# Kernel optimization log

Hardware: AMD Instinct MI355X
Metric: run time of the kernel (lower is better)

Reference implementation:

```python
import jax, jax.numpy as jnp
import numpy as np

B, N0, C, H, T = 32, 513, 768, 12, 10
Dh = C // H
SCALE = Dh ** -0.5
HID = 4 * C  # mlp hidden


def _ln(x, g, b, eps=1e-5):
    m = jnp.mean(x, axis=-1, keepdims=True)
    v = jnp.mean((x - m) ** 2, axis=-1, keepdims=True)
    return (x - m) * jax.lax.rsqrt(v + eps) * g + b


def setup_inputs() -> dict:
    key = jax.random.key(0)
    ks = jax.random.split(key, 8)
    s = 0.02
    return {
        "x": jax.random.normal(ks[0], (B, N0, C), jnp.float32),
        "global_feature": jax.random.normal(ks[1], (B, 1, C), jnp.float32),
        "token_position": jax.random.normal(ks[2], (T, C), jnp.float32) * s,
        "prompt_emb": jax.random.normal(ks[3], (T, C), jnp.float32) * s,
        "scaler1": jnp.ones((1,), jnp.float32) * 0.3,
        "g1": jnp.ones((C,), jnp.float32),
        "b1": jnp.zeros((C,), jnp.float32),
        "w_qkv": jax.random.normal(ks[4], (3 * C, C), jnp.float32) * s,
        "w_proj": jax.random.normal(ks[5], (C, C), jnp.float32) * s,
        "b_proj": jnp.zeros((C,), jnp.float32),
        "g2": jnp.ones((C,), jnp.float32),
        "b2": jnp.zeros((C,), jnp.float32),
        "w_fc1": jax.random.normal(ks[6], (HID, C), jnp.float32) * s,
        "b_fc1": jnp.zeros((HID,), jnp.float32),
        "w_fc2": jax.random.normal(ks[7], (C, HID), jnp.float32) * s,
        "b_fc2": jnp.zeros((C,), jnp.float32),
    }


def reference(x, global_feature, token_position, prompt_emb, scaler1,
              g1, b1, w_qkv, w_proj, b_proj, g2, b2,
              w_fc1, b_fc1, w_fc2, b_fc2):
    # prompt-token fusion: [1,T,C] + [B,1,C] + [1,T,C] -> [B,T,C]
    token_prompt = prompt_emb[None] + scaler1 * global_feature + token_position[None]
    x = jnp.concatenate([x[:, :1], token_prompt, x[:, 1:]], axis=1)  # [B, N, C]
    Bx, N, _ = x.shape

    # attention branch
    h = _ln(x, g1, b1)
    qkv = h @ w_qkv.T  # [B, N, 3C]
    qkv = qkv.reshape(Bx, N, 3, H, Dh)
    q = qkv[:, :, 0].transpose(0, 2, 1, 3)  # [B, H, N, Dh]
    k = qkv[:, :, 1].transpose(0, 2, 1, 3)
    v = qkv[:, :, 2].transpose(0, 2, 1, 3)
    attn = jax.nn.softmax(jnp.einsum('bhqd,bhkd->bhqk', q, k) * SCALE, axis=-1)
    o = jnp.einsum('bhqk,bhkd->bhqd', attn, v).transpose(0, 2, 1, 3).reshape(Bx, N, C)
    x = x + o @ w_proj.T + b_proj

    # mlp branch (exact GELU as nn.GELU)
    h2 = _ln(x, g2, b2)
    x = x + jax.nn.gelu(h2 @ w_fc1.T + b_fc1, approximate=False) @ w_fc2.T + b_fc2
    return x
```

## Files before the change

kernel.cpp:

```cpp
#include <hip/hip_runtime.h>
#include <math.h>

typedef float  f32x4 __attribute__((ext_vector_type(4)));
typedef short  s16x8 __attribute__((ext_vector_type(8)));
typedef unsigned short u16;

#define DEVI static __device__ __forceinline__

constexpr int B_   = 32, N0_ = 513, C_ = 768, H_ = 12, T_ = 10;
constexpr int NSEQ = 523;
constexpr int M_   = B_ * NSEQ;
constexpr int HID_ = 3072;
constexpr float SCALE_ = 0.125f;
constexpr int NPAD = 576;

constexpr size_t OFF_A  = 25706496;
constexpr size_t OFF_VT = OFF_A + 77119488;
constexpr size_t OFF_O  = OFF_VT + 28311552;
constexpr size_t OFF_W  = OFF_O + 25706496;
constexpr size_t OFF_WQ = OFF_W;
constexpr size_t OFF_WP = OFF_WQ + 3538944;
constexpr size_t OFF_W1 = OFF_WP + 1179648;
constexpr size_t OFF_W2 = OFF_W1 + 4718592;

DEVI u16 f2bf(float f) {
  union { float f; unsigned u; } x; x.f = f;
  unsigned r = x.u + 0x7fffu + ((x.u >> 16) & 1u);
  return (u16)(r >> 16);
}

DEVI void async_ld16(const void* g, void* l) {
  __builtin_amdgcn_global_load_lds(
      (const __attribute__((address_space(1))) unsigned*)g,
      (__attribute__((address_space(3))) unsigned*)l, 16, 0, 0);
}

DEVI f32x4 mfma16(s16x8 a, s16x8 b, f32x4 c) {
  return __builtin_amdgcn_mfma_f32_16x16x32_bf16(a, b, c, 0, 0, 0);
}

__global__ void k_cvt(const float* __restrict__ in, u16* __restrict__ out, int n4) {
  int i = blockIdx.x * 256 + threadIdx.x;
  if (i >= n4) return;
  float4 v = reinterpret_cast<const float4*>(in)[i];
  ushort4 o;
  o.x = f2bf(v.x); o.y = f2bf(v.y); o.z = f2bf(v.z); o.w = f2bf(v.w);
  reinterpret_cast<ushort4*>(out)[i] = o;
}

__global__ void k_build(const float* __restrict__ x, const float* __restrict__ gf,
                        const float* __restrict__ tp, const float* __restrict__ pe,
                        const float* __restrict__ s1, float* __restrict__ xcat) {
  int i = blockIdx.x * 256 + threadIdx.x;
  if (i >= M_ * C_ / 4) return;
  int row = i / (C_ / 4), c4 = i % (C_ / 4);
  int b = row / NSEQ, n = row - b * NSEQ;
  float4 v;
  if (n == 0) {
    v = reinterpret_cast<const float4*>(x + (size_t)b * N0_ * C_)[c4];
  } else if (n <= T_) {
    int t = n - 1;
    float4 a  = reinterpret_cast<const float4*>(pe + (size_t)t * C_)[c4];
    float4 tv = reinterpret_cast<const float4*>(tp + (size_t)t * C_)[c4];
    float4 g  = reinterpret_cast<const float4*>(gf + (size_t)b * C_)[c4];
    float s = s1[0];
    v.x = a.x + s * g.x + tv.x; v.y = a.y + s * g.y + tv.y;
    v.z = a.z + s * g.z + tv.z; v.w = a.w + s * g.w + tv.w;
  } else {
    v = reinterpret_cast<const float4*>(x + ((size_t)b * N0_ + (n - T_)) * C_)[c4];
  }
  reinterpret_cast<float4*>(xcat + (size_t)row * C_)[c4] = v;
}

__global__ void k_ln(const float* __restrict__ xin, const float* __restrict__ g,
                     const float* __restrict__ bb, u16* __restrict__ hout) {
  int lane = threadIdx.x & 63, wid = threadIdx.x >> 6;
  int row = blockIdx.x * 4 + wid;
  const float4* xr = reinterpret_cast<const float4*>(xin + (size_t)row * C_);
  float4 v[3]; float s = 0.f, sq = 0.f;
#pragma unroll
  for (int c = 0; c < 3; ++c) {
    v[c] = xr[c * 64 + lane];
    s  += v[c].x + v[c].y + v[c].z + v[c].w;
    sq += v[c].x * v[c].x + v[c].y * v[c].y + v[c].z * v[c].z + v[c].w * v[c].w;
  }
#pragma unroll
  for (int m = 1; m < 64; m <<= 1) { s += __shfl_xor(s, m, 64); sq += __shfl_xor(sq, m, 64); }
  float mean = s * (1.f / C_);
  float rstd = rsqrtf(sq * (1.f / C_) - mean * mean + 1e-5f);
  ushort4* orow = reinterpret_cast<ushort4*>(hout + (size_t)row * C_);
#pragma unroll
  for (int c = 0; c < 3; ++c) {
    float4 gv = reinterpret_cast<const float4*>(g)[c * 64 + lane];
    float4 bv = reinterpret_cast<const float4*>(bb)[c * 64 + lane];
    ushort4 o;
    o.x = f2bf((v[c].x - mean) * rstd * gv.x + bv.x);
    o.y = f2bf((v[c].y - mean) * rstd * gv.y + bv.y);
    o.z = f2bf((v[c].z - mean) * rstd * gv.z + bv.z);
    o.w = f2bf((v[c].w - mean) * rstd * gv.w + bv.w);
    orow[c * 64 + lane] = o;
  }
}

template<int EPI, int NDIM, int KDIM>
__global__ __launch_bounds__(256) void k_gemm(
    const u16* __restrict__ A, const u16* __restrict__ Bw,
    u16* __restrict__ outb, float* __restrict__ outf,
    const float* __restrict__ bias, const float* __restrict__ resid,
    u16* __restrict__ vT) {
  __shared__ __align__(16) char lds[32768];
  const int m0 = blockIdx.x * 128, n0 = blockIdx.y * 128;
  const int lane = threadIdx.x & 63, wid = threadIdx.x >> 6;
  const int wr = wid >> 1, wc = wid & 1;
  f32x4 acc[4][4] = {};

  for (int k0 = 0; k0 < KDIM; k0 += 64) {
    __syncthreads();
#pragma unroll
    for (int jj = 0; jj < 4; ++jj) {
      int j = wid * 4 + jj;
      int row = j * 8 + (lane >> 3);
      int gm = m0 + row; if (gm > M_ - 1) gm = M_ - 1;
      int cb = ((lane & 7) * 16) ^ ((row & 7) << 4);
      async_ld16((const char*)A + ((size_t)gm * KDIM + k0) * 2 + cb, lds + j * 1024);
    }
#pragma unroll
    for (int jj = 0; jj < 4; ++jj) {
      int j = wid * 4 + jj;
      int row = j * 8 + (lane >> 3);
      int cb = ((lane & 7) * 16) ^ ((row & 7) << 4);
      async_ld16((const char*)Bw + ((size_t)(n0 + row) * KDIM + k0) * 2 + cb,
                 lds + 16384 + j * 1024);
    }
    __syncthreads();
#pragma unroll
    for (int kk = 0; kk < 2; ++kk) {
      s16x8 af[4], bfr[4];
#pragma unroll
      for (int i = 0; i < 4; ++i) {
        int row = wr * 64 + i * 16 + (lane & 15);
        int cb = (kk * 64 + (lane >> 4) * 16) ^ ((row & 7) << 4);
        af[i] = *reinterpret_cast<const s16x8*>(lds + row * 128 + cb);
      }
#pragma unroll
      for (int j = 0; j < 4; ++j) {
        int row = wc * 64 + j * 16 + (lane & 15);
        int cb = (kk * 64 + (lane >> 4) * 16) ^ ((row & 7) << 4);
        bfr[j] = *reinterpret_cast<const s16x8*>(lds + 16384 + row * 128 + cb);
      }
#pragma unroll
      for (int i = 0; i < 4; ++i)
#pragma unroll
        for (int j = 0; j < 4; ++j)
          acc[i][j] = mfma16(af[i], bfr[j], acc[i][j]);
    }
  }

#pragma unroll
  for (int i = 0; i < 4; ++i) {
#pragma unroll
    for (int j = 0; j < 4; ++j) {
#pragma unroll
      for (int r = 0; r < 4; ++r) {
        int gm = m0 + wr * 64 + i * 16 + (lane >> 4) * 4 + r;
        int gn = n0 + wc * 64 + j * 16 + (lane & 15);
        if (gm < M_) {
          float v = acc[i][j][r];
          if constexpr (EPI == 0) {
            u16 bv = f2bf(v);
            outb[(size_t)gm * NDIM + gn] = bv;
            if (gn >= 2 * C_) {
              int hh = (gn - 2 * C_) >> 6;
              int dh = gn & 63;
              int b2 = gm / NSEQ, nn = gm - b2 * NSEQ;
              vT[((size_t)(b2 * H_ + hh) * 64 + dh) * NPAD + nn] = bv;
            }
          } else if constexpr (EPI == 1) {
            size_t idx = (size_t)gm * NDIM + gn;
            outf[idx] = v + bias[gn] + resid[idx];
          } else {
            float t = v + bias[gn];
            outb[(size_t)gm * NDIM + gn] =
                f2bf(0.5f * t * (1.f + erff(t * 0.70710678118654752f)));
          }
        }
      }
    }
  }
}

__global__ __launch_bounds__(256) void k_attn(const u16* __restrict__ qkv,
                                              const u16* __restrict__ vT,
                                              u16* __restrict__ o) {
  __shared__ __align__(16) char lds[24576];
  const int qt = blockIdx.x, bh = blockIdx.y;
  const int b = bh / H_, h = bh - b * H_;
  const int lane = threadIdx.x & 63, wid = threadIdx.x >> 6;

  s16x8 qf[2];
  {
    int n = qt * 64 + wid * 16 + (lane & 15); if (n > NSEQ - 1) n = NSEQ - 1;
    const u16* qrow = qkv + (size_t)(b * NSEQ + n) * (3 * C_) + h * 64 + (lane >> 4) * 8;
    qf[0] = *reinterpret_cast<const s16x8*>(qrow);
    qf[1] = *reinterpret_cast<const s16x8*>(qrow + 32);
  }
  float m_run[4] = {-1e30f, -1e30f, -1e30f, -1e30f};
  float l_run[4] = {0.f, 0.f, 0.f, 0.f};
  f32x4 oacc[4] = {};
  char* pl = lds + 16384 + wid * 2048;

  for (int t = 0; t < 9; ++t) {
    const int kv0 = t * 64;
    __syncthreads();
#pragma unroll
    for (int jj = 0; jj < 2; ++jj) {
      int j = wid * 2 + jj;
      int row = j * 8 + (lane >> 3);
      int n = kv0 + row; if (n > NSEQ - 1) n = NSEQ - 1;
      int cb = ((lane & 7) * 16) ^ ((row & 7) << 4);
      async_ld16((const char*)(qkv + (size_t)(b * NSEQ + n) * (3 * C_) + C_ + h * 64) + cb,
                 lds + j * 1024);
    }
#pragma unroll
    for (int jj = 0; jj < 2; ++jj) {
      int j = wid * 2 + jj;
      int dh = j * 8 + (lane >> 3);
      int cb = ((lane & 7) * 16) ^ ((dh & 7) << 4);
      async_ld16((const char*)(vT + ((size_t)bh * 64 + dh) * NPAD + kv0) + cb,
                 lds + 8192 + j * 1024);
    }
    __syncthreads();

    f32x4 sfr[4] = {};
#pragma unroll
    for (int kk = 0; kk < 2; ++kk) {
#pragma unroll
      for (int fc = 0; fc < 4; ++fc) {
        int row = fc * 16 + (lane & 15);
        int cb = (kk * 64 + (lane >> 4) * 16) ^ ((row & 7) << 4);
        s16x8 kf = *reinterpret_cast<const s16x8*>(lds + row * 128 + cb);
        sfr[fc] = mfma16(qf[kk], kf, sfr[fc]);
      }
    }
#pragma unroll
    for (int fc = 0; fc < 4; ++fc) {
      bool valid = (kv0 + fc * 16 + (lane & 15)) < NSEQ;
#pragma unroll
      for (int r = 0; r < 4; ++r)
        sfr[fc][r] = valid ? sfr[fc][r] * SCALE_ : -1e30f;
    }
#pragma unroll
    for (int r = 0; r < 4; ++r) {
      float mx = fmaxf(fmaxf(sfr[0][r], sfr[1][r]), fmaxf(sfr[2][r], sfr[3][r]));
      mx = fmaxf(mx, __shfl_xor(mx, 1, 64));
      mx = fmaxf(mx, __shfl_xor(mx, 2, 64));
      mx = fmaxf(mx, __shfl_xor(mx, 4, 64));
      mx = fmaxf(mx, __shfl_xor(mx, 8, 64));
      float mnew = fmaxf(m_run[r], mx);
      float sc = __expf(m_run[r] - mnew);
      l_run[r] *= sc;
#pragma unroll
      for (int f2 = 0; f2 < 4; ++f2) oacc[f2][r] *= sc;
      float ps = 0.f;
#pragma unroll
      for (int fc = 0; fc < 4; ++fc) {
        float p = __expf(sfr[fc][r] - mnew);
        sfr[fc][r] = p; ps += p;
      }
      ps += __shfl_xor(ps, 1, 64);
      ps += __shfl_xor(ps, 2, 64);
      ps += __shfl_xor(ps, 4, 64);
      ps += __shfl_xor(ps, 8, 64);
      l_run[r] += ps;
      m_run[r] = mnew;
    }
#pragma unroll
    for (int fc = 0; fc < 4; ++fc)
#pragma unroll
      for (int r = 0; r < 4; ++r) {
        int row = (lane >> 4) * 4 + r;
        int cb = ((fc * 16 + (lane & 15)) * 2) ^ ((row & 7) << 4);
        *reinterpret_cast<u16*>(pl + row * 128 + cb) = f2bf(sfr[fc][r]);
      }
    s16x8 pf[2];
#pragma unroll
    for (int ks = 0; ks < 2; ++ks) {
      int row = lane & 15;
      int cb = (ks * 64 + (lane >> 4) * 16) ^ ((row & 7) << 4);
      pf[ks] = *reinterpret_cast<const s16x8*>(pl + row * 128 + cb);
    }
#pragma unroll
    for (int f2 = 0; f2 < 4; ++f2)
#pragma unroll
      for (int ks = 0; ks < 2; ++ks) {
        int vrow = f2 * 16 + (lane & 15);
        int cb = (ks * 64 + (lane >> 4) * 16) ^ ((vrow & 7) << 4);
        s16x8 vf = *reinterpret_cast<const s16x8*>(lds + 8192 + vrow * 128 + cb);
        oacc[f2] = mfma16(pf[ks], vf, oacc[f2]);
      }
  }
#pragma unroll
  for (int f2 = 0; f2 < 4; ++f2)
#pragma unroll
    for (int r = 0; r < 4; ++r) {
      int n = qt * 64 + wid * 16 + (lane >> 4) * 4 + r;
      if (n < NSEQ) {
        float val = oacc[f2][r] / l_run[r];
        o[(size_t)(b * NSEQ + n) * C_ + h * 64 + f2 * 16 + (lane & 15)] = f2bf(val);
      }
    }
}

extern "C" void kernel_launch(void* const* d_in, const int* in_sizes, int n_in,
                              void* d_out, int out_size, void* d_ws, size_t ws_size,
                              hipStream_t stream) {
  const float* x    = (const float*)d_in[0];
  const float* gf   = (const float*)d_in[1];
  const float* tp   = (const float*)d_in[2];
  const float* pe   = (const float*)d_in[3];
  const float* s1   = (const float*)d_in[4];
  const float* g1   = (const float*)d_in[5];
  const float* b1   = (const float*)d_in[6];
  const float* wqkv = (const float*)d_in[7];
  const float* wproj= (const float*)d_in[8];
  const float* bproj= (const float*)d_in[9];
  const float* g2   = (const float*)d_in[10];
  const float* b2   = (const float*)d_in[11];
  const float* wfc1 = (const float*)d_in[12];
  const float* bfc1 = (const float*)d_in[13];
  const float* wfc2 = (const float*)d_in[14];
  const float* bfc2 = (const float*)d_in[15];

  char* ws = (char*)d_ws;
  u16* h    = (u16*)ws;
  u16* qkvb = (u16*)(ws + OFF_A);
  u16* hmid = qkvb;
  u16* vTb  = (u16*)(ws + OFF_VT);
  u16* ob   = (u16*)(ws + OFF_O);
  u16* wqb  = (u16*)(ws + OFF_WQ);
  u16* wpb  = (u16*)(ws + OFF_WP);
  u16* w1b  = (u16*)(ws + OFF_W1);
  u16* w2b  = (u16*)(ws + OFF_W2);
  float* xcat = (float*)d_out;

  k_cvt<<<(442368 + 255) / 256, 256, 0, stream>>>(wqkv, wqb, 442368);
  k_cvt<<<(147456 + 255) / 256, 256, 0, stream>>>(wproj, wpb, 147456);
  k_cvt<<<(589824 + 255) / 256, 256, 0, stream>>>(wfc1, w1b, 589824);
  k_cvt<<<(589824 + 255) / 256, 256, 0, stream>>>(wfc2, w2b, 589824);

  k_build<<<(M_ * C_ / 4 + 255) / 256, 256, 0, stream>>>(x, gf, tp, pe, s1, xcat);
  k_ln<<<M_ / 4, 256, 0, stream>>>(xcat, g1, b1, h);
  k_gemm<0, 2304, 768><<<dim3(131, 18), 256, 0, stream>>>(h, wqb, qkvb, nullptr, nullptr, nullptr, vTb);
  k_attn<<<dim3(9, B_ * H_), 256, 0, stream>>>(qkvb, vTb, ob);
  k_gemm<1, 768, 768><<<dim3(131, 6), 256, 0, stream>>>(ob, wpb, nullptr, xcat, bproj, xcat, nullptr);
  k_ln<<<M_ / 4, 256, 0, stream>>>(xcat, g2, b2, h);
  k_gemm<2, 3072, 768><<<dim3(131, 24), 256, 0, stream>>>(h, w1b, hmid, nullptr, bfc1, nullptr, nullptr);
  k_gemm<1, 768, 3072><<<dim3(131, 6), 256, 0, stream>>>(hmid, w2b, nullptr, (float*)d_out, bfc2, xcat, nullptr);
}
```

Measured before the change: 882.9 us.

## Enlarge GEMM tiles, double-buffer LDS, and remap workgroups across XCDs

The GEMM kernel now uses templated 256x256 or 256x128 tiles with 512 threads (8 waves), replacing 128x128 tiles with 256 threads. It double-buffers the K-loop in dynamic shared memory so the next tile's global-to-LDS load overlaps the current MFMA work, and it maps workgroup IDs so consecutive tiles land on the same XCD. The goal is more data reuse per loaded tile, hidden memory latency and better L2 locality. The costs are more LDS and registers per block, fewer blocks in flight, and less even wave balance on the tail.

```diff
diff --git a/kernel.cpp b/kernel.cpp
--- a/kernel.cpp
+++ b/kernel.cpp
@@ -102,70 +102,94 @@
   }
 }
 
-template<int EPI, int NDIM, int KDIM>
-__global__ __launch_bounds__(256) void k_gemm(
+template<int EPI, int NDIM, int KDIM, int BM, int BN>
+__global__ __launch_bounds__(512, 2) void k_gemm(
     const u16* __restrict__ A, const u16* __restrict__ Bw,
     u16* __restrict__ outb, float* __restrict__ outf,
     const float* __restrict__ bias, const float* __restrict__ resid,
     u16* __restrict__ vT) {
-  __shared__ __align__(16) char lds[32768];
-  const int m0 = blockIdx.x * 128, n0 = blockIdx.y * 128;
+  extern __shared__ __align__(16) char smem[];
+  constexpr int NMB  = (M_ + BM - 1) / BM;
+  constexpr int MI   = BM / 32;
+  constexpr int NJ   = BN / 64;
+  constexpr int BUFB = (BM + BN) * 128;
+  constexpr int NT   = KDIM / 64;
+
   const int lane = threadIdx.x & 63, wid = threadIdx.x >> 6;
-  const int wr = wid >> 1, wc = wid & 1;
-  f32x4 acc[4][4] = {};
-
-  for (int k0 = 0; k0 < KDIM; k0 += 64) {
-    __syncthreads();
-#pragma unroll
-    for (int jj = 0; jj < 4; ++jj) {
-      int j = wid * 4 + jj;
+  const int wr = wid >> 2, wc = wid & 3;
+
+  const int nwg = gridDim.x;
+  const int q = nwg >> 3, r = nwg & 7;
+  const int xcd = blockIdx.x & 7, sub = blockIdx.x >> 3;
+  const int wgid = (xcd < r ? xcd * (q + 1) : r * (q + 1) + (xcd - r) * q) + sub;
+  const int nb = wgid / NMB, mb = wgid - nb * NMB;
+  const int m0 = mb * BM, n0 = nb * BN;
+
+  auto stage = [&](int buf, int k0) {
+    char* la = smem + buf * BUFB;
+    char* lb = la + BM * 128;
+#pragma unroll
+    for (int jj = 0; jj < BM / 64; ++jj) {
+      int j = jj * 8 + wid;
       int row = j * 8 + (lane >> 3);
       int gm = m0 + row; if (gm > M_ - 1) gm = M_ - 1;
       int cb = ((lane & 7) * 16) ^ ((row & 7) << 4);
-      async_ld16((const char*)A + ((size_t)gm * KDIM + k0) * 2 + cb, lds + j * 1024);
-    }
-#pragma unroll
-    for (int jj = 0; jj < 4; ++jj) {
-      int j = wid * 4 + jj;
+      async_ld16((const char*)A + ((size_t)gm * KDIM + k0) * 2 + cb, la + j * 1024);
+    }
+#pragma unroll
+    for (int jj = 0; jj < BN / 64; ++jj) {
+      int j = jj * 8 + wid;
       int row = j * 8 + (lane >> 3);
       int cb = ((lane & 7) * 16) ^ ((row & 7) << 4);
       async_ld16((const char*)Bw + ((size_t)(n0 + row) * KDIM + k0) * 2 + cb,
-                 lds + 16384 + j * 1024);
+                 lb + j * 1024);
+    }
+  };
+
+  f32x4 acc[MI][NJ] = {};
+  stage(0, 0);
+  __syncthreads();
+  int cur = 0;
+#pragma unroll 1
+  for (int t = 0; t < NT; ++t) {
+    if (t + 1 < NT) stage(cur ^ 1, (t + 1) * 64);
+    const char* la = smem + cur * BUFB;
+    const char* lb = la + BM * 128;
+#pragma unroll
+    for (int kk = 0; kk < 2; ++kk) {
+      s16x8 af[MI], bfr[NJ];
+#pragma unroll
+      for (int ii = 0; ii < MI; ++ii) {
+        int row = wr * (BM / 2) + ii * 16 + (lane & 15);
+        int cb = (kk * 64 + (lane >> 4) * 16) ^ ((row & 7) << 4);
+        af[ii] = *reinterpret_cast<const s16x8*>(la + row * 128 + cb);
+      }
+#pragma unroll
+      for (int jj = 0; jj < NJ; ++jj) {
+        int row = wc * (BN / 4) + jj * 16 + (lane & 15);
+        int cb = (kk * 64 + (lane >> 4) * 16) ^ ((row & 7) << 4);
+        bfr[jj] = *reinterpret_cast<const s16x8*>(lb + row * 128 + cb);
+      }
+#pragma unroll
+      for (int ii = 0; ii < MI; ++ii)
+#pragma unroll
+        for (int jj = 0; jj < NJ; ++jj)
+          acc[ii][jj] = mfma16(af[ii], bfr[jj], acc[ii][jj]);
     }
     __syncthreads();
-#pragma unroll
-    for (int kk = 0; kk < 2; ++kk) {
-      s16x8 af[4], bfr[4];
-#pragma unroll
-      for (int i = 0; i < 4; ++i) {
-        int row = wr * 64 + i * 16 + (lane & 15);
-        int cb = (kk * 64 + (lane >> 4) * 16) ^ ((row & 7) << 4);
-        af[i] = *reinterpret_cast<const s16x8*>(lds + row * 128 + cb);
-      }
-#pragma unroll
-      for (int j = 0; j < 4; ++j) {
-        int row = wc * 64 + j * 16 + (lane & 15);
-        int cb = (kk * 64 + (lane >> 4) * 16) ^ ((row & 7) << 4);
-        bfr[j] = *reinterpret_cast<const s16x8*>(lds + 16384 + row * 128 + cb);
-      }
-#pragma unroll
-      for (int i = 0; i < 4; ++i)
-#pragma unroll
-        for (int j = 0; j < 4; ++j)
-          acc[i][j] = mfma16(af[i], bfr[j], acc[i][j]);
-    }
-  }
-
-#pragma unroll
-  for (int i = 0; i < 4; ++i) {
-#pragma unroll
-    for (int j = 0; j < 4; ++j) {
-#pragma unroll
-      for (int r = 0; r < 4; ++r) {
-        int gm = m0 + wr * 64 + i * 16 + (lane >> 4) * 4 + r;
-        int gn = n0 + wc * 64 + j * 16 + (lane & 15);
+    cur ^= 1;
+  }
+
+#pragma unroll
+  for (int ii = 0; ii < MI; ++ii) {
+#pragma unroll
+    for (int jj = 0; jj < NJ; ++jj) {
+#pragma unroll
+      for (int rr = 0; rr < 4; ++rr) {
+        int gm = m0 + wr * (BM / 2) + ii * 16 + (lane >> 4) * 4 + rr;
+        int gn = n0 + wc * (BN / 4) + jj * 16 + (lane & 15);
         if (gm < M_) {
-          float v = acc[i][j][r];
+          float v = acc[ii][jj][rr];
           if constexpr (EPI == 0) {
             u16 bv = f2bf(v);
             outb[(size_t)gm * NDIM + gn] = bv;
@@ -246,41 +270,41 @@
     for (int fc = 0; fc < 4; ++fc) {
       bool valid = (kv0 + fc * 16 + (lane & 15)) < NSEQ;
 #pragma unroll
-      for (int r = 0; r < 4; ++r)
-        sfr[fc][r] = valid ? sfr[fc][r] * SCALE_ : -1e30f;
-    }
-#pragma unroll
-    for (int r = 0; r < 4; ++r) {
-      float mx = fmaxf(fmaxf(sfr[0][r], sfr[1][r]), fmaxf(sfr[2][r], sfr[3][r]));
+      for (int rr = 0; rr < 4; ++rr)
+        sfr[fc][rr] = valid ? sfr[fc][rr] * SCALE_ : -1e30f;
+    }
+#pragma unroll
+    for (int rr = 0; rr < 4; ++rr) {
+      float mx = fmaxf(fmaxf(sfr[0][rr], sfr[1][rr]), fmaxf(sfr[2][rr], sfr[3][rr]));
       mx = fmaxf(mx, __shfl_xor(mx, 1, 64));
       mx = fmaxf(mx, __shfl_xor(mx, 2, 64));
       mx = fmaxf(mx, __shfl_xor(mx, 4, 64));
       mx = fmaxf(mx, __shfl_xor(mx, 8, 64));
-      float mnew = fmaxf(m_run[r], mx);
-      float sc = __expf(m_run[r] - mnew);
-      l_run[r] *= sc;
-#pragma unroll
-      for (int f2 = 0; f2 < 4; ++f2) oacc[f2][r] *= sc;
+      float mnew = fmaxf(m_run[rr], mx);
+      float sc = __expf(m_run[rr] - mnew);
+      l_run[rr] *= sc;
+#pragma unroll
+      for (int f2 = 0; f2 < 4; ++f2) oacc[f2][rr] *= sc;
       float ps = 0.f;
 #pragma unroll
       for (int fc = 0; fc < 4; ++fc) {
-        float p = __expf(sfr[fc][r] - mnew);
-        sfr[fc][r] = p; ps += p;
+        float p = __expf(sfr[fc][rr] - mnew);
+        sfr[fc][rr] = p; ps += p;
       }
       ps += __shfl_xor(ps, 1, 64);
       ps += __shfl_xor(ps, 2, 64);
       ps += __shfl_xor(ps, 4, 64);
       ps += __shfl_xor(ps, 8, 64);
-      l_run[r] += ps;
-      m_run[r] = mnew;
+      l_run[rr] += ps;
+      m_run[rr] = mnew;
     }
 #pragma unroll
     for (int fc = 0; fc < 4; ++fc)
 #pragma unroll
-      for (int r = 0; r < 4; ++r) {
-        int row = (lane >> 4) * 4 + r;
+      for (int rr = 0; rr < 4; ++rr) {
+        int row = (lane >> 4) * 4 + rr;
         int cb = ((fc * 16 + (lane & 15)) * 2) ^ ((row & 7) << 4);
-        *reinterpret_cast<u16*>(pl + row * 128 + cb) = f2bf(sfr[fc][r]);
+        *reinterpret_cast<u16*>(pl + row * 128 + cb) = f2bf(sfr[fc][rr]);
       }
     s16x8 pf[2];
 #pragma unroll
@@ -302,10 +326,10 @@
 #pragma unroll
   for (int f2 = 0; f2 < 4; ++f2)
 #pragma unroll
-    for (int r = 0; r < 4; ++r) {
-      int n = qt * 64 + wid * 16 + (lane >> 4) * 4 + r;
+    for (int rr = 0; rr < 4; ++rr) {
+      int n = qt * 64 + wid * 16 + (lane >> 4) * 4 + rr;
       if (n < NSEQ) {
-        float val = oacc[f2][r] / l_run[r];
+        float val = oacc[f2][rr] / l_run[rr];
         o[(size_t)(b * NSEQ + n) * C_ + h * 64 + f2 * 16 + (lane & 15)] = f2bf(val);
       }
     }
@@ -343,6 +367,17 @@
   u16* w2b  = (u16*)(ws + OFF_W2);
   float* xcat = (float*)d_out;
 
+  constexpr int SH256 = (256 + 256) * 128 * 2;
+  constexpr int SH128 = (256 + 128) * 128 * 2;
+  (void)hipFuncSetAttribute((const void*)&k_gemm<0, 2304, 768, 256, 256>,
+      hipFuncAttributeMaxDynamicSharedMemorySize, SH256);
+  (void)hipFuncSetAttribute((const void*)&k_gemm<2, 3072, 768, 256, 256>,
+      hipFuncAttributeMaxDynamicSharedMemorySize, SH256);
+  (void)hipFuncSetAttribute((const void*)&k_gemm<1, 768, 768, 256, 128>,
+      hipFuncAttributeMaxDynamicSharedMemorySize, SH128);
+  (void)hipFuncSetAttribute((const void*)&k_gemm<1, 768, 3072, 256, 128>,
+      hipFuncAttributeMaxDynamicSharedMemorySize, SH128);
+
   k_cvt<<<(442368 + 255) / 256, 256, 0, stream>>>(wqkv, wqb, 442368);
   k_cvt<<<(147456 + 255) / 256, 256, 0, stream>>>(wproj, wpb, 147456);
   k_cvt<<<(589824 + 255) / 256, 256, 0, stream>>>(wfc1, w1b, 589824);
@@ -350,10 +385,14 @@
 
   k_build<<<(M_ * C_ / 4 + 255) / 256, 256, 0, stream>>>(x, gf, tp, pe, s1, xcat);
   k_ln<<<M_ / 4, 256, 0, stream>>>(xcat, g1, b1, h);
-  k_gemm<0, 2304, 768><<<dim3(131, 18), 256, 0, stream>>>(h, wqb, qkvb, nullptr, nullptr, nullptr, vTb);
+  k_gemm<0, 2304, 768, 256, 256><<<66 * 9, 512, SH256, stream>>>(
+      h, wqb, qkvb, nullptr, nullptr, nullptr, vTb);
   k_attn<<<dim3(9, B_ * H_), 256, 0, stream>>>(qkvb, vTb, ob);
-  k_gemm<1, 768, 768><<<dim3(131, 6), 256, 0, stream>>>(ob, wpb, nullptr, xcat, bproj, xcat, nullptr);
+  k_gemm<1, 768, 768, 256, 128><<<66 * 6, 512, SH128, stream>>>(
+      ob, wpb, nullptr, xcat, bproj, xcat, nullptr);
   k_ln<<<M_ / 4, 256, 0, stream>>>(xcat, g2, b2, h);
-  k_gemm<2, 3072, 768><<<dim3(131, 24), 256, 0, stream>>>(h, w1b, hmid, nullptr, bfc1, nullptr, nullptr);
-  k_gemm<1, 768, 3072><<<dim3(131, 6), 256, 0, stream>>>(hmid, w2b, nullptr, (float*)d_out, bfc2, xcat, nullptr);
-}
+  k_gemm<2, 3072, 768, 256, 256><<<66 * 12, 512, SH256, stream>>>(
+      h, w1b, hmid, nullptr, bfc1, nullptr, nullptr);
+  k_gemm<1, 768, 3072, 256, 128><<<66 * 6, 512, SH128, stream>>>(
+      hmid, w2b, nullptr, (float*)d_out, bfc2, xcat, nullptr);
+}
```

Result: faster. 850.8 us (-3.6%).
